# Kernel tuning notes

Hardware: AMD Instinct MI355X
Metric: run time of the kernel (lower is better)

## Reference

```python
import jax, jax.numpy as jnp
import numpy as np

N = 100_000      # num nodes
E = 100_000      # num hyperedges
NNZ = 1_600_000  # incidence entries (avg degree 16)
DIN = 128
DOUT = 128


def setup_inputs() -> dict:
    key = jax.random.key(0)
    k1, k2, k3, k4 = jax.random.split(key, 4)
    x = jax.random.normal(k1, (N, DIN), dtype=jnp.float32)
    weight = jax.random.normal(k2, (DIN, DOUT), dtype=jnp.float32) / np.sqrt(DIN).astype(np.float32)
    bias = jax.random.normal(k3, (DOUT,), dtype=jnp.float32) * 0.02
    hyperedge_index = jax.random.randint(k4, (2, NNZ), 0, N, dtype=jnp.int64)
    return {"x": x, "weight": weight, "bias": bias, "hyperedge_index": hyperedge_index}


def reference(x, weight, bias, hyperedge_index):
    # PyG HypergraphConv (use_attention=False, heads=1):
    #   out = D^{-1} H W B^{-1} H^T (x @ Theta) + bias, W = I (unit hyperedge weights)
    node_idx = hyperedge_index[0]  # [NNZ]
    edge_idx = hyperedge_index[1]  # [NNZ]

    h = x @ weight  # [N, DOUT]

    ones = jnp.ones((NNZ,), dtype=h.dtype)
    # node degree D_i = sum of hyperedge weights (=1) over incident hyperedges
    D = jax.ops.segment_sum(ones, node_idx, num_segments=N)   # [N]
    # hyperedge degree B_e = number of incident nodes
    B = jax.ops.segment_sum(ones, edge_idx, num_segments=E)   # [E]
    Dinv = jnp.where(D > 0, 1.0 / D, 0.0)
    Binv = jnp.where(B > 0, 1.0 / B, 0.0)

    # nodes -> hyperedges: m_e = B_e^{-1} * sum_{i in e} h_i
    e_feat = jax.ops.segment_sum(h[node_idx], edge_idx, num_segments=E) * Binv[:, None]  # [E, DOUT]
    # hyperedges -> nodes: out_i = D_i^{-1} * sum_{e ni i} m_e
    out = jax.ops.segment_sum(e_feat[edge_idx], node_idx, num_segments=N) * Dinv[:, None]  # [N, DOUT]
    return out + bias
```

## Files before the change

kernel.cpp:

```cpp
#include <hip/hip_runtime.h>

#define Nn 100000
#define Ne 100000
#define NNZC 1600000
#define NBLK 256
#define CHUNK 6250
#define BSH 8
#define BUCKW 256
#define NBK 391
#define GEMM_TOTAL 1563
#define GEMM_A 782
#define GEMM_B 781
#define FCAP 5888
#define SEGW 4

typedef __attribute__((ext_vector_type(8))) short short8;
typedef __attribute__((ext_vector_type(4))) float floatx4;

__device__ inline unsigned short f2bf(float f) {
    union { float f; unsigned int i; } c; c.f = f;
    unsigned int i = c.i;
    return (unsigned short)((i + 0x7fffu + ((i >> 16) & 1u)) >> 16);
}
__device__ inline unsigned int f2bf2(float lo, float hi) {
    union { float f; unsigned int i; } a, b;
    a.f = lo; b.f = hi;
    const unsigned int x = (a.i + 0x7fffu + ((a.i >> 16) & 1u)) >> 16;
    const unsigned int y = (b.i + 0x7fffu + ((b.i >> 16) & 1u)) & 0xffff0000u;
    return x | y;
}

union FusedLds {
    unsigned short wlds[128 * 136];
    struct { int a[NBK]; int b[NBK]; } s;
};

__device__ inline void gemm_block(int gb, const float* __restrict__ x,
                                  const float* __restrict__ w,
                                  unsigned short* __restrict__ h,
                                  unsigned short* wlds, int tid) {
    const int wave = tid >> 6, lane = tid & 63;
    const int q = lane >> 4, r16 = lane & 15;

    for (int i = tid; i < 4096; i += 256) {
        const int k = i >> 5;
        const int n0 = (i & 31) << 2;
        const float4 wv = *(const float4*)(w + k * 128 + n0);
        wlds[(n0 + 0) * 136 + k] = f2bf(wv.x);
        wlds[(n0 + 1) * 136 + k] = f2bf(wv.y);
        wlds[(n0 + 2) * 136 + k] = f2bf(wv.z);
        wlds[(n0 + 3) * 136 + k] = f2bf(wv.w);
    }
    __syncthreads();

    const int row0 = gb * 64 + wave * 16;
    const int rrow = min(row0 + r16, Nn - 1);

    floatx4 acc[8];
#pragma unroll
    for (int jb = 0; jb < 8; ++jb) acc[jb] = (floatx4){0.f, 0.f, 0.f, 0.f};

    const float* ap = x + (size_t)rrow * 128 + q * 8;
#pragma unroll
    for (int kk = 0; kk < 4; ++kk) {
        const float4 a0 = *(const float4*)(ap + kk * 32);
        const float4 a1 = *(const float4*)(ap + kk * 32 + 4);
        union { unsigned int u[4]; short8 s; } xf;
        xf.u[0] = f2bf2(a0.x, a0.y);
        xf.u[1] = f2bf2(a0.z, a0.w);
        xf.u[2] = f2bf2(a1.x, a1.y);
        xf.u[3] = f2bf2(a1.z, a1.w);
        const unsigned short* wp = wlds + kk * 32 + q * 8;
#pragma unroll
        for (int jb = 0; jb < 8; ++jb) {
            const short8 wf = *(const short8*)(wp + (jb * 16 + r16) * 136);
            acc[jb] = __builtin_amdgcn_mfma_f32_16x16x32_bf16(wf, xf.s, acc[jb], 0, 0, 0);
        }
    }

    if (row0 + r16 < Nn) {
        unsigned short* hb = h + (size_t)(row0 + r16) * 128 + q * 4;
#pragma unroll
        for (int jb = 0; jb < 8; ++jb) {
            uint2 o;
            o.x = f2bf2(acc[jb][0], acc[jb][1]);
            o.y = f2bf2(acc[jb][2], acc[jb][3]);
            *(uint2*)(hb + jb * 16) = o;
        }
    }
}

__global__ __launch_bounds__(256) void hist_gemm_kernel(
        const int* __restrict__ nidx, const int* __restrict__ eidx,
        int* __restrict__ histN, int* __restrict__ histE,
        const float* __restrict__ x, const float* __restrict__ w,
        unsigned short* __restrict__ h) {
    __shared__ FusedLds sm;
    const int tid = threadIdx.x;
    if (blockIdx.x < NBLK) {
        for (int j = tid; j < NBK; j += 256) { sm.s.a[j] = 0; sm.s.b[j] = 0; }
        __syncthreads();
        const int base = blockIdx.x * CHUNK;
        for (int i = base + tid; i < base + CHUNK; i += 256) {
            atomicAdd(&sm.s.a[nidx[i] >> BSH], 1);
            atomicAdd(&sm.s.b[eidx[i] >> BSH], 1);
        }
        __syncthreads();
        for (int j = tid; j < NBK; j += 256) {
            histN[j * NBLK + blockIdx.x] = sm.s.a[j];
            histE[j * NBLK + blockIdx.x] = sm.s.b[j];
        }
    } else {
        gemm_block(blockIdx.x - NBLK, x, w, h, sm.wlds, tid);
    }
}

__global__ void scan1_kernel(int* __restrict__ histN, int* __restrict__ histE,
                             int* __restrict__ bsumN, int* __restrict__ bsumE) {
    const int arr = blockIdx.x / NBK;
    const int b = blockIdx.x % NBK;
    int* a = arr ? histE : histN;
    int* bs = arr ? bsumE : bsumN;
    const int t = threadIdx.x;
    int v = a[b * 256 + t];
    __shared__ int tmp[2][256];
    int pin = 0;
    tmp[0][t] = v;
    for (int off = 1; off < 256; off <<= 1) {
        __syncthreads();
        int val = tmp[pin][t];
        if (t >= off) val += tmp[pin][t - off];
        tmp[1 - pin][t] = val;
        pin ^= 1;
    }
    __syncthreads();
    int incl = tmp[pin][t];
    a[b * 256 + t] = incl - v;
    if (t == 255) bs[b] = incl;
}

__global__ void scan3_kernel(int* __restrict__ histN, int* __restrict__ histE,
                             const int* __restrict__ bsumN, const int* __restrict__ bsumE) {
    const int arr = blockIdx.x / NBK;
    const int b = blockIdx.x % NBK;
    int* a = arr ? histE : histN;
    const int* bs = arr ? bsumE : bsumN;
    const int t = threadIdx.x;
    int part = 0;
    for (int i = t; i < b; i += 256) part += bs[i];
    __shared__ int red[256];
    red[t] = part;
    __syncthreads();
    for (int off = 128; off > 0; off >>= 1) {
        if (t < off) red[t] += red[t + off];
        __syncthreads();
    }
    a[b * 256 + t] += red[0];
}

__global__ __launch_bounds__(256) void scatter_gemm_kernel(
        const int* __restrict__ nidx, const int* __restrict__ eidx,
        const int* __restrict__ histN, const int* __restrict__ histE,
        unsigned int* __restrict__ pairsN, unsigned int* __restrict__ pairsE,
        const float* __restrict__ x, const float* __restrict__ w,
        unsigned short* __restrict__ h) {
    __shared__ FusedLds sm;
    const int tid = threadIdx.x;
    if (blockIdx.x < NBLK) {
        const int blk = blockIdx.x;
        for (int j = tid; j < NBK; j += 256) {
            sm.s.a[j] = histN[j * NBLK + blk];
            sm.s.b[j] = histE[j * NBLK + blk];
        }
        __syncthreads();
        const int base = blk * CHUNK;
        for (int i = base + tid; i < base + CHUNK; i += 256) {
            const int n = nidx[i], e = eidx[i];
            const int pn = atomicAdd(&sm.s.a[n >> BSH], 1);
            const int pe = atomicAdd(&sm.s.b[e >> BSH], 1);
            pairsN[pn] = ((unsigned int)e << 8) | (unsigned int)(n & 255);
            pairsE[pe] = ((unsigned int)n << 8) | (unsigned int)(e & 255);
        }
    } else {
        gemm_block(GEMM_A + blockIdx.x - NBLK, x, w, h, sm.wlds, tid);
    }
}

__global__ void fine_kernel(const unsigned int* __restrict__ pairsN, const unsigned int* __restrict__ pairsE,
                            const int* __restrict__ histN, const int* __restrict__ histE,
                            int* __restrict__ offsN, int* __restrict__ offsE,
                            int* __restrict__ permN, int* __restrict__ permE) {
    const int arr = blockIdx.x / NBK;
    const int b = blockIdx.x % NBK;
    const unsigned int* pairs = arr ? pairsE : pairsN;
    const int* hist = arr ? histE : histN;
    int* offs = arr ? offsE : offsN;
    int* perm = arr ? permE : permN;
    const int t = threadIdx.x;
    const int S = hist[b * NBLK];
    const int E = (b + 1 < NBK) ? hist[(b + 1) * NBLK] : NNZC;
    __shared__ int cnt[BUCKW];
    __shared__ int tmp[2][BUCKW];
    __shared__ unsigned int cache[FCAP];
    cnt[t] = 0;
    __syncthreads();
    for (int i = S + t; i < E; i += BUCKW) {
        const unsigned int p = pairs[i];
        const int loc = i - S;
        if (loc < FCAP) cache[loc] = p;
        atomicAdd(&cnt[p & 255u], 1);
    }
    __syncthreads();
    int v = cnt[t];
    int pin = 0;
    tmp[0][t] = v;
    for (int off = 1; off < BUCKW; off <<= 1) {
        __syncthreads();
        int val = tmp[pin][t];
        if (t >= off) val += tmp[pin][t - off];
        tmp[1 - pin][t] = val;
        pin ^= 1;
    }
    __syncthreads();
    const int excl = tmp[pin][t] - v;
    const int id = b * BUCKW + t;
    if (id < 100000) offs[id] = S + excl;
    if (b == NBK - 1 && t == 0) offs[100000] = NNZC;
    __syncthreads();
    cnt[t] = excl;
    __syncthreads();
    for (int i = S + t; i < E; i += BUCKW) {
        const int loc = i - S;
        const unsigned int p = (loc < FCAP) ? cache[loc] : pairs[i];
        const int pos = S + atomicAdd(&cnt[p & 255u], 1);
        perm[pos] = (int)(p >> 8);
    }
}

template <int MODE>
__global__ __launch_bounds__(256) void gather_seg_kernel(
        const int* __restrict__ perm, const int* __restrict__ offs,
        const void* __restrict__ srcv, const float* __restrict__ bias,
        void* __restrict__ outv) {
    const int wave = threadIdx.x >> 6;
    const int lane = threadIdx.x & 63;
    const int e0 = __builtin_amdgcn_readfirstlane((blockIdx.x * 4 + wave) * SEGW);
    const int start = offs[e0];
    const int end = offs[e0 + SEGW];
    const unsigned int laneoff = (unsigned int)lane << 2;
    const char* src = (const char*)srcv;

    float bx = 0.f, by = 0.f;
    if (MODE == 1) {
        const float2 b = ((const float2*)bias)[lane];
        bx = b.x; by = b.y;
    }

    float ax = 0.f, ay = 0.f;
    int e = e0;
    int seg_start = start;
    int nb = offs[e0 + 1];

    auto flush = [&](int deg) {
        const float sinv = deg ? 1.f / (float)deg : 0.f;
        if (MODE == 0) {
            *(unsigned int*)((char*)outv + (((unsigned int)e << 8) | laneoff)) =
                f2bf2(ax * sinv, ay * sinv);
        } else {
            float2 o;
            o.x = ax * sinv + bx;
            o.y = ay * sinv + by;
            *(float2*)((char*)outv + (((unsigned int)e << 9) | (laneoff << 1))) = o;
        }
        ax = 0.f; ay = 0.f;
        ++e;
    };

    int myv = 0;
    for (int i = start; i < end; i += 8) {
        const int t = (i - start) & 63;
        if (t == 0) myv = perm[min(i + lane, NNZC - 1)];
        const int m = min(end - i, 8);
        unsigned int a[8], u[8];
#pragma unroll
        for (int j = 0; j < 8; ++j)
            a[j] = ((unsigned int)__shfl(myv, t + (j < m ? j : m - 1), 64) << 8) | laneoff;
#pragma unroll
        for (int j = 0; j < 8; ++j) u[j] = *(const unsigned int*)(src + a[j]);
#pragma unroll
        for (int j = 0; j < 8; ++j) {
            if (j < m) {
                while (i + j == nb) {
                    flush(nb - seg_start);
                    seg_start = nb;
                    nb = offs[e + 1];
                }
                ax += __uint_as_float(u[j] << 16);
                ay += __uint_as_float(u[j] & 0xffff0000u);
            }
        }
    }
    while (e < e0 + SEGW) {
        flush(end - seg_start);
        seg_start = end;
    }
}

extern "C" void kernel_launch(void* const* d_in, const int* in_sizes, int n_in,
                              void* d_out, int out_size, void* d_ws, size_t ws_size,
                              hipStream_t stream) {
    const float* x = (const float*)d_in[0];
    const float* w = (const float*)d_in[1];
    const float* bias = (const float*)d_in[2];
    const int* hei = (const int*)d_in[3];
    const int* nidx = hei;
    const int* eidx = hei + NNZC;
    float* out = (float*)d_out;

    char* p = (char*)d_ws;
    unsigned short* h = (unsigned short*)p;  p += (size_t)Nn * 128 * 2;
    unsigned short* ef = (unsigned short*)p; p += (size_t)Ne * 128 * 2;
    int* histN = (int*)p;                    p += (size_t)NBK * NBLK * 4 + 256;
    int* histE = (int*)p;                    p += (size_t)NBK * NBLK * 4 + 256;
    int* bsumN = (int*)p;                    p += 1792;
    int* bsumE = (int*)p;                    p += 1792;
    int* offsN = (int*)p;                    p += 400128;
    int* offsE = (int*)p;                    p += 400128;
    int* permN = (int*)p;                    p += (size_t)NNZC * 4;
    int* permE = (int*)p;                    p += (size_t)NNZC * 4;
    unsigned int* pairsN = (unsigned int*)p; p += (size_t)NNZC * 4;
    unsigned int* pairsE = (unsigned int*)p; p += (size_t)NNZC * 4;

    hist_gemm_kernel<<<NBLK + GEMM_A, 256, 0, stream>>>(nidx, eidx, histN, histE, x, w, h);
    scan1_kernel<<<2 * NBK, 256, 0, stream>>>(histN, histE, bsumN, bsumE);
    scan3_kernel<<<2 * NBK, 256, 0, stream>>>(histN, histE, bsumN, bsumE);
    scatter_gemm_kernel<<<NBLK + GEMM_B, 256, 0, stream>>>(nidx, eidx, histN, histE,
                                                           pairsN, pairsE, x, w, h);
    fine_kernel<<<2 * NBK, BUCKW, 0, stream>>>(pairsN, pairsE, histN, histE,
                                               offsN, offsE, permN, permE);

    gather_seg_kernel<0><<<Ne / (4 * SEGW), 256, 0, stream>>>(permE, offsE, h, nullptr, ef);
    gather_seg_kernel<1><<<Nn / (4 * SEGW), 256, 0, stream>>>(permN, offsN, ef, bias, out);
}
```

Measured before the change: 311.3 us.

## Pipeline gather-segment row loads through LDS with async global_load_lds ring

Reworks the gather/segment-sum kernel so each wave issues direct global-to-LDS loads (global_load_lds) for upcoming batches of 8 gathered rows into a 4-slot per-wave LDS ring. It keeps two batches in flight and waits with explicit vmcnt before reading the oldest slot. Segment offsets are loaded once into scalars instead of being re-read during accumulation, and the next chunk of the permutation is prefetched. The goal is to hide gather latency with deeper memory-level parallelism. In exchange it adds 32 KB of LDS per block, which may reduce occupancy, and relies on hand-written waitcnt ordering.

```diff
diff --git a/kernel.cpp b/kernel.cpp
--- a/kernel.cpp
+++ b/kernel.cpp
@@ -16,6 +16,8 @@
 
 typedef __attribute__((ext_vector_type(8))) short short8;
 typedef __attribute__((ext_vector_type(4))) float floatx4;
+typedef __attribute__((address_space(1))) const unsigned int gu32;
+typedef __attribute__((address_space(3))) unsigned int lu32;
 
 __device__ inline unsigned short f2bf(float f) {
     union { float f; unsigned int i; } c; c.f = f;
@@ -242,24 +244,55 @@
         const int* __restrict__ perm, const int* __restrict__ offs,
         const void* __restrict__ srcv, const float* __restrict__ bias,
         void* __restrict__ outv) {
+    __shared__ unsigned int ring[4][4][8][64];
     const int wave = threadIdx.x >> 6;
     const int lane = threadIdx.x & 63;
     const int e0 = __builtin_amdgcn_readfirstlane((blockIdx.x * 4 + wave) * SEGW);
-    const int start = offs[e0];
-    const int end = offs[e0 + SEGW];
+
+    const int o0 = __builtin_amdgcn_readfirstlane(offs[e0]);
+    const int o1 = __builtin_amdgcn_readfirstlane(offs[e0 + 1]);
+    const int o2 = __builtin_amdgcn_readfirstlane(offs[e0 + 2]);
+    const int o3 = __builtin_amdgcn_readfirstlane(offs[e0 + 3]);
+    const int o4 = __builtin_amdgcn_readfirstlane(offs[e0 + 4]);
+    const int start = o0, end = o4;
+    const int nrows = end - start;
+    const int nbatch = (nrows + 7) >> 3;
+
     const unsigned int laneoff = (unsigned int)lane << 2;
     const char* src = (const char*)srcv;
 
     float bx = 0.f, by = 0.f;
-    if (MODE == 1) {
-        const float2 b = ((const float2*)bias)[lane];
-        bx = b.x; by = b.y;
-    }
+    if (MODE == 1) { const float2 b = ((const float2*)bias)[lane]; bx = b.x; by = b.y; }
+
+    int cur = perm[min(start + lane, NNZC - 1)];
+    int nxt = perm[min(start + 64 + lane, NNZC - 1)];
+    int wbase = 0;
+
+    unsigned int* const myring = &ring[wave][0][0][0];
+
+    auto issue = [&](int b) {
+        const int rel0 = b << 3;
+        if ((rel0 >> 6) > wbase) {
+            cur = nxt;
+            ++wbase;
+            nxt = perm[min(start + ((wbase + 1) << 6) + lane, NNZC - 1)];
+        }
+        const int rbase = rel0 & 63;
+        const int relmax = nrows - 1 - (wbase << 6);
+        unsigned int* lslot = myring + ((b & 3) << 9);
+#pragma unroll
+        for (int j = 0; j < 8; ++j) {
+            const int k = min(rbase + j, relmax);
+            const unsigned int rid = (unsigned int)__shfl(cur, k, 64);
+            const char* g = src + (((unsigned long long)rid << 8) | laneoff);
+            __builtin_amdgcn_global_load_lds((gu32*)g, (lu32*)(lslot + (j << 6)), 4, 0, 0);
+        }
+    };
 
     float ax = 0.f, ay = 0.f;
     int e = e0;
     int seg_start = start;
-    int nb = offs[e0 + 1];
+    int nb = o1;
 
     auto flush = [&](int deg) {
         const float sinv = deg ? 1.f / (float)deg : 0.f;
@@ -275,30 +308,48 @@
         ax = 0.f; ay = 0.f;
         ++e;
     };
-
-    int myv = 0;
-    for (int i = start; i < end; i += 8) {
-        const int t = (i - start) & 63;
-        if (t == 0) myv = perm[min(i + lane, NNZC - 1)];
+    auto nextnb = [&]() {
+        const int k = e - e0;
+        return k == 0 ? o1 : k == 1 ? o2 : k == 2 ? o3 : o4;
+    };
+
+    auto accumulate = [&](int t, const unsigned int* u) {
+        const int i = start + (t << 3);
         const int m = min(end - i, 8);
-        unsigned int a[8], u[8];
-#pragma unroll
-        for (int j = 0; j < 8; ++j)
-            a[j] = ((unsigned int)__shfl(myv, t + (j < m ? j : m - 1), 64) << 8) | laneoff;
-#pragma unroll
-        for (int j = 0; j < 8; ++j) u[j] = *(const unsigned int*)(src + a[j]);
 #pragma unroll
         for (int j = 0; j < 8; ++j) {
             if (j < m) {
                 while (i + j == nb) {
                     flush(nb - seg_start);
                     seg_start = nb;
-                    nb = offs[e + 1];
+                    nb = nextnb();
                 }
                 ax += __uint_as_float(u[j] << 16);
                 ay += __uint_as_float(u[j] & 0xffff0000u);
             }
         }
+    };
+
+    if (nbatch > 0) issue(0);
+    if (nbatch > 1) issue(1);
+
+    for (int t = 0; t + 1 < nbatch; ++t) {
+        asm volatile("s_waitcnt vmcnt(8)" ::: "memory");
+        const unsigned int* lslot = myring + ((t & 3) << 9);
+        unsigned int u[8];
+#pragma unroll
+        for (int j = 0; j < 8; ++j) u[j] = lslot[(j << 6) + lane];
+        if (t + 2 < nbatch) issue(t + 2);
+        accumulate(t, u);
+    }
+    if (nbatch > 0) {
+        asm volatile("s_waitcnt vmcnt(0)" ::: "memory");
+        const int t = nbatch - 1;
+        const unsigned int* lslot = myring + ((t & 3) << 9);
+        unsigned int u[8];
+#pragma unroll
+        for (int j = 0; j < 8; ++j) u[j] = lslot[(j << 6) + lane];
+        accumulate(t, u);
     }
     while (e < e0 + SEGW) {
         flush(end - seg_start);
```

Result: slower. 406.8 us (+30.7%).

## Replace two-level radix CSR build with global atomic counting sort

Applied to the files above, without the earlier changes.

Replaces the coarse-bucket histogram, pair scatter and per-bucket fine sort with a direct counting sort: global atomics count the degree of each node and hyperedge, a two-pass scan turns the counts into offsets, and a second pass of global atomics scatters the neighbor ids straight into CSR order. This drops the fine_kernel launch and the pairs intermediate buffers. In exchange it issues 3.2M global atomics spread over random addresses, on top of a memset, and the order of entries within a segment becomes nondeterministic, which can slightly change floating-point summation order.

```diff
diff --git a/kernel.cpp b/kernel.cpp
--- a/kernel.cpp
+++ b/kernel.cpp
@@ -5,13 +5,10 @@
 #define NNZC 1600000
 #define NBLK 256
 #define CHUNK 6250
-#define BSH 8
-#define BUCKW 256
 #define NBK 391
 #define GEMM_TOTAL 1563
 #define GEMM_A 782
 #define GEMM_B 781
-#define FCAP 5888
 #define SEGW 4
 
 typedef __attribute__((ext_vector_type(8))) short short8;
@@ -29,11 +26,6 @@
     const unsigned int y = (b.i + 0x7fffu + ((b.i >> 16) & 1u)) & 0xffff0000u;
     return x | y;
 }
-
-union FusedLds {
-    unsigned short wlds[128 * 136];
-    struct { int a[NBK]; int b[NBK]; } s;
-};
 
 __device__ inline void gemm_block(int gb, const float* __restrict__ x,
                                   const float* __restrict__ w,
@@ -90,39 +82,35 @@
     }
 }
 
-__global__ __launch_bounds__(256) void hist_gemm_kernel(
+__global__ __launch_bounds__(256) void count_gemm_kernel(
         const int* __restrict__ nidx, const int* __restrict__ eidx,
-        int* __restrict__ histN, int* __restrict__ histE,
+        int* __restrict__ cntN, int* __restrict__ cntE,
         const float* __restrict__ x, const float* __restrict__ w,
         unsigned short* __restrict__ h) {
-    __shared__ FusedLds sm;
+    __shared__ unsigned short wlds[128 * 136];
     const int tid = threadIdx.x;
     if (blockIdx.x < NBLK) {
-        for (int j = tid; j < NBK; j += 256) { sm.s.a[j] = 0; sm.s.b[j] = 0; }
-        __syncthreads();
         const int base = blockIdx.x * CHUNK;
         for (int i = base + tid; i < base + CHUNK; i += 256) {
-            atomicAdd(&sm.s.a[nidx[i] >> BSH], 1);
-            atomicAdd(&sm.s.b[eidx[i] >> BSH], 1);
-        }
-        __syncthreads();
-        for (int j = tid; j < NBK; j += 256) {
-            histN[j * NBLK + blockIdx.x] = sm.s.a[j];
-            histE[j * NBLK + blockIdx.x] = sm.s.b[j];
+            atomicAdd(&cntN[nidx[i]], 1);
+            atomicAdd(&cntE[eidx[i]], 1);
         }
     } else {
-        gemm_block(blockIdx.x - NBLK, x, w, h, sm.wlds, tid);
-    }
-}
-
-__global__ void scan1_kernel(int* __restrict__ histN, int* __restrict__ histE,
+        gemm_block(blockIdx.x - NBLK, x, w, h, wlds, tid);
+    }
+}
+
+__global__ void scanA_kernel(const int* __restrict__ cntN, const int* __restrict__ cntE,
+                             int* __restrict__ offsN, int* __restrict__ offsE,
                              int* __restrict__ bsumN, int* __restrict__ bsumE) {
     const int arr = blockIdx.x / NBK;
     const int b = blockIdx.x % NBK;
-    int* a = arr ? histE : histN;
+    const int* c = arr ? cntE : cntN;
+    int* o = arr ? offsE : offsN;
     int* bs = arr ? bsumE : bsumN;
     const int t = threadIdx.x;
-    int v = a[b * 256 + t];
+    const int id = b * 256 + t;
+    const int v = (id < 100000) ? c[id] : 0;
     __shared__ int tmp[2][256];
     int pin = 0;
     tmp[0][t] = v;
@@ -134,16 +122,18 @@
         pin ^= 1;
     }
     __syncthreads();
-    int incl = tmp[pin][t];
-    a[b * 256 + t] = incl - v;
+    const int incl = tmp[pin][t];
+    if (id < 100000) o[id] = incl - v;
     if (t == 255) bs[b] = incl;
 }
 
-__global__ void scan3_kernel(int* __restrict__ histN, int* __restrict__ histE,
+__global__ void scanB_kernel(int* __restrict__ offsN, int* __restrict__ offsE,
+                             int* __restrict__ curN, int* __restrict__ curE,
                              const int* __restrict__ bsumN, const int* __restrict__ bsumE) {
     const int arr = blockIdx.x / NBK;
     const int b = blockIdx.x % NBK;
-    int* a = arr ? histE : histN;
+    int* o = arr ? offsE : offsN;
+    int* cu = arr ? curE : curN;
     const int* bs = arr ? bsumE : bsumN;
     const int t = threadIdx.x;
     int part = 0;
@@ -155,85 +145,34 @@
         if (t < off) red[t] += red[t + off];
         __syncthreads();
     }
-    a[b * 256 + t] += red[0];
+    const int id = b * 256 + t;
+    if (id < 100000) {
+        const int val = o[id] + red[0];
+        o[id] = val;
+        cu[id] = val;
+    }
+    if (b == NBK - 1 && t == 0) o[100000] = NNZC;
 }
 
 __global__ __launch_bounds__(256) void scatter_gemm_kernel(
         const int* __restrict__ nidx, const int* __restrict__ eidx,
-        const int* __restrict__ histN, const int* __restrict__ histE,
-        unsigned int* __restrict__ pairsN, unsigned int* __restrict__ pairsE,
+        int* __restrict__ curN, int* __restrict__ curE,
+        int* __restrict__ permN, int* __restrict__ permE,
         const float* __restrict__ x, const float* __restrict__ w,
         unsigned short* __restrict__ h) {
-    __shared__ FusedLds sm;
+    __shared__ unsigned short wlds[128 * 136];
     const int tid = threadIdx.x;
     if (blockIdx.x < NBLK) {
-        const int blk = blockIdx.x;
-        for (int j = tid; j < NBK; j += 256) {
-            sm.s.a[j] = histN[j * NBLK + blk];
-            sm.s.b[j] = histE[j * NBLK + blk];
-        }
-        __syncthreads();
-        const int base = blk * CHUNK;
+        const int base = blockIdx.x * CHUNK;
         for (int i = base + tid; i < base + CHUNK; i += 256) {
             const int n = nidx[i], e = eidx[i];
-            const int pn = atomicAdd(&sm.s.a[n >> BSH], 1);
-            const int pe = atomicAdd(&sm.s.b[e >> BSH], 1);
-            pairsN[pn] = ((unsigned int)e << 8) | (unsigned int)(n & 255);
-            pairsE[pe] = ((unsigned int)n << 8) | (unsigned int)(e & 255);
+            const int pn = atomicAdd(&curN[n], 1);
+            permN[pn] = e;
+            const int pe = atomicAdd(&curE[e], 1);
+            permE[pe] = n;
         }
     } else {
-        gemm_block(GEMM_A + blockIdx.x - NBLK, x, w, h, sm.wlds, tid);
-    }
-}
-
-__global__ void fine_kernel(const unsigned int* __restrict__ pairsN, const unsigned int* __restrict__ pairsE,
-                            const int* __restrict__ histN, const int* __restrict__ histE,
-                            int* __restrict__ offsN, int* __restrict__ offsE,
-                            int* __restrict__ permN, int* __restrict__ permE) {
-    const int arr = blockIdx.x / NBK;
-    const int b = blockIdx.x % NBK;
-    const unsigned int* pairs = arr ? pairsE : pairsN;
-    const int* hist = arr ? histE : histN;
-    int* offs = arr ? offsE : offsN;
-    int* perm = arr ? permE : permN;
-    const int t = threadIdx.x;
-    const int S = hist[b * NBLK];
-    const int E = (b + 1 < NBK) ? hist[(b + 1) * NBLK] : NNZC;
-    __shared__ int cnt[BUCKW];
-    __shared__ int tmp[2][BUCKW];
-    __shared__ unsigned int cache[FCAP];
-    cnt[t] = 0;
-    __syncthreads();
-    for (int i = S + t; i < E; i += BUCKW) {
-        const unsigned int p = pairs[i];
-        const int loc = i - S;
-        if (loc < FCAP) cache[loc] = p;
-        atomicAdd(&cnt[p & 255u], 1);
-    }
-    __syncthreads();
-    int v = cnt[t];
-    int pin = 0;
-    tmp[0][t] = v;
-    for (int off = 1; off < BUCKW; off <<= 1) {
-        __syncthreads();
-        int val = tmp[pin][t];
-        if (t >= off) val += tmp[pin][t - off];
-        tmp[1 - pin][t] = val;
-        pin ^= 1;
-    }
-    __syncthreads();
-    const int excl = tmp[pin][t] - v;
-    const int id = b * BUCKW + t;
-    if (id < 100000) offs[id] = S + excl;
-    if (b == NBK - 1 && t == 0) offs[100000] = NNZC;
-    __syncthreads();
-    cnt[t] = excl;
-    __syncthreads();
-    for (int i = S + t; i < E; i += BUCKW) {
-        const int loc = i - S;
-        const unsigned int p = (loc < FCAP) ? cache[loc] : pairs[i];
-        const int pos = S + atomicAdd(&cnt[p & 255u], 1);
-        perm[pos] = (int)(p >> 8);
+        gemm_block(GEMM_A + blockIdx.x - NBLK, x, w, h, wlds, tid);
     }
 }
 
@@ -320,24 +259,23 @@
     char* p = (char*)d_ws;
     unsigned short* h = (unsigned short*)p;  p += (size_t)Nn * 128 * 2;
     unsigned short* ef = (unsigned short*)p; p += (size_t)Ne * 128 * 2;
-    int* histN = (int*)p;                    p += (size_t)NBK * NBLK * 4 + 256;
-    int* histE = (int*)p;                    p += (size_t)NBK * NBLK * 4 + 256;
+    int* cntN = (int*)p;                     p += 400384;
+    int* cntE = (int*)p;                     p += 400384;
     int* bsumN = (int*)p;                    p += 1792;
     int* bsumE = (int*)p;                    p += 1792;
-    int* offsN = (int*)p;                    p += 400128;
-    int* offsE = (int*)p;                    p += 400128;
+    int* offsN = (int*)p;                    p += 400384;
+    int* offsE = (int*)p;                    p += 400384;
+    int* curN = (int*)p;                     p += 400384;
+    int* curE = (int*)p;                     p += 400384;
     int* permN = (int*)p;                    p += (size_t)NNZC * 4;
     int* permE = (int*)p;                    p += (size_t)NNZC * 4;
-    unsigned int* pairsN = (unsigned int*)p; p += (size_t)NNZC * 4;
-    unsigned int* pairsE = (unsigned int*)p; p += (size_t)NNZC * 4;
-
-    hist_gemm_kernel<<<NBLK + GEMM_A, 256, 0, stream>>>(nidx, eidx, histN, histE, x, w, h);
-    scan1_kernel<<<2 * NBK, 256, 0, stream>>>(histN, histE, bsumN, bsumE);
-    scan3_kernel<<<2 * NBK, 256, 0, stream>>>(histN, histE, bsumN, bsumE);
-    scatter_gemm_kernel<<<NBLK + GEMM_B, 256, 0, stream>>>(nidx, eidx, histN, histE,
-                                                           pairsN, pairsE, x, w, h);
-    fine_kernel<<<2 * NBK, BUCKW, 0, stream>>>(pairsN, pairsE, histN, histE,
-                                               offsN, offsE, permN, permE);
+
+    hipMemsetAsync(cntN, 0, 2 * 400384, stream);
+    count_gemm_kernel<<<NBLK + GEMM_A, 256, 0, stream>>>(nidx, eidx, cntN, cntE, x, w, h);
+    scanA_kernel<<<2 * NBK, 256, 0, stream>>>(cntN, cntE, offsN, offsE, bsumN, bsumE);
+    scanB_kernel<<<2 * NBK, 256, 0, stream>>>(offsN, offsE, curN, curE, bsumN, bsumE);
+    scatter_gemm_kernel<<<NBLK + GEMM_B, 256, 0, stream>>>(nidx, eidx, curN, curE,
+                                                           permN, permE, x, w, h);
 
     gather_seg_kernel<0><<<Ne / (4 * SEGW), 256, 0, stream>>>(permE, offsE, h, nullptr, ef);
     gather_seg_kernel<1><<<Nn / (4 * SEGW), 256, 0, stream>>>(permN, offsN, ef, bias, out);
```

After: 604.2 us. 1.94x slower.

## Split GEMM into three parts and co-schedule fine sort with GEMM and gather

Applied to the files above, without the earlier changes.

The GEMM blocks are now spread across three kernels. A third slice runs alongside the hyperedge-side fine sort. The node-side fine sort now runs inside the same launch as the first gather (nodes to hyperedges) instead of in its own kernel before both gathers. This fills idle CUs during the low-parallelism fine-sort phase and removes one launch. In exchange, the LDS cache capacity (FCAP) shrinks so the combined LDS union fits. This may raise global re-reads for large buckets and changes block scheduling balance.

```diff
diff --git a/kernel.cpp b/kernel.cpp
--- a/kernel.cpp
+++ b/kernel.cpp
@@ -9,10 +9,12 @@
 #define BUCKW 256
 #define NBK 391
 #define GEMM_TOTAL 1563
-#define GEMM_A 782
-#define GEMM_B 781
-#define FCAP 5888
+#define GEMM_A 600
+#define GEMM_B 600
+#define GEMM_C 363
+#define FCAP 4608
 #define SEGW 4
+#define NG0 6250
 
 typedef __attribute__((ext_vector_type(8))) short short8;
 typedef __attribute__((ext_vector_type(4))) float floatx4;
@@ -33,6 +35,15 @@
 union FusedLds {
     unsigned short wlds[128 * 136];
     struct { int a[NBK]; int b[NBK]; } s;
+};
+struct FineLds {
+    int cnt[BUCKW];
+    int tmp[2][BUCKW];
+    unsigned int cache[FCAP];
+};
+union FineGemmLds {
+    unsigned short wlds[128 * 136];
+    FineLds f;
 };
 
 __device__ inline void gemm_block(int gb, const float* __restrict__ x,
@@ -87,6 +98,117 @@
             o.y = f2bf2(acc[jb][2], acc[jb][3]);
             *(uint2*)(hb + jb * 16) = o;
         }
+    }
+}
+
+__device__ inline void fine_block(int b, const unsigned int* __restrict__ pairs,
+                                  const int* __restrict__ hist,
+                                  int* __restrict__ offs, int* __restrict__ perm,
+                                  FineLds& L, int t) {
+    const int S = hist[b * NBLK];
+    const int E = (b + 1 < NBK) ? hist[(b + 1) * NBLK] : NNZC;
+    L.cnt[t] = 0;
+    __syncthreads();
+    for (int i = S + t; i < E; i += BUCKW) {
+        const unsigned int p = pairs[i];
+        const int loc = i - S;
+        if (loc < FCAP) L.cache[loc] = p;
+        atomicAdd(&L.cnt[p & 255u], 1);
+    }
+    __syncthreads();
+    int v = L.cnt[t];
+    int pin = 0;
+    L.tmp[0][t] = v;
+    for (int off = 1; off < BUCKW; off <<= 1) {
+        __syncthreads();
+        int val = L.tmp[pin][t];
+        if (t >= off) val += L.tmp[pin][t - off];
+        L.tmp[1 - pin][t] = val;
+        pin ^= 1;
+    }
+    __syncthreads();
+    const int excl = L.tmp[pin][t] - v;
+    const int id = b * BUCKW + t;
+    if (id < 100000) offs[id] = S + excl;
+    if (b == NBK - 1 && t == 0) offs[100000] = NNZC;
+    __syncthreads();
+    L.cnt[t] = excl;
+    __syncthreads();
+    for (int i = S + t; i < E; i += BUCKW) {
+        const int loc = i - S;
+        const unsigned int p = (loc < FCAP) ? L.cache[loc] : pairs[i];
+        const int pos = S + atomicAdd(&L.cnt[p & 255u], 1);
+        perm[pos] = (int)(p >> 8);
+    }
+}
+
+template <int MODE>
+__device__ inline void gather_body(int gblk, const int* __restrict__ perm,
+                                   const int* __restrict__ offs,
+                                   const void* __restrict__ srcv,
+                                   const float* __restrict__ bias,
+                                   void* __restrict__ outv, int tid) {
+    const int wave = tid >> 6;
+    const int lane = tid & 63;
+    const int e0 = __builtin_amdgcn_readfirstlane((gblk * 4 + wave) * SEGW);
+    const int start = offs[e0];
+    const int end = offs[e0 + SEGW];
+    const unsigned int laneoff = (unsigned int)lane << 2;
+    const char* src = (const char*)srcv;
+
+    float bx = 0.f, by = 0.f;
+    if (MODE == 1) {
+        const float2 b = ((const float2*)bias)[lane];
+        bx = b.x; by = b.y;
+    }
+
+    float ax = 0.f, ay = 0.f;
+    int e = e0;
+    int seg_start = start;
+    int nb = offs[e0 + 1];
+
+    auto flush = [&](int deg) {
+        const float sinv = deg ? 1.f / (float)deg : 0.f;
+        if (MODE == 0) {
+            *(unsigned int*)((char*)outv + (((unsigned int)e << 8) | laneoff)) =
+                f2bf2(ax * sinv, ay * sinv);
+        } else {
+            float2 o;
+            o.x = ax * sinv + bx;
+            o.y = ay * sinv + by;
+            *(float2*)((char*)outv + (((unsigned int)e << 9) | (laneoff << 1))) = o;
+        }
+        ax = 0.f; ay = 0.f;
+        ++e;
+    };
+
+    int myv = 0;
+    for (int i = start; i < end; i += 8) {
+        const int t = (i - start) & 63;
+        if (t == 0) myv = perm[min(i + lane, NNZC - 1)];
+        const int m = min(end - i, 8);
+        unsigned int a[8], u[8];
+#pragma unroll
+        for (int j = 0; j < 8; ++j)
+            a[j] = ((unsigned int)__shfl(myv, t + (j < m ? j : m - 1), 64) << 8) | laneoff;
+#pragma unroll
+        for (int j = 0; j < 8; ++j) u[j] = *(const unsigned int*)(src + a[j]);
+#pragma unroll
+        for (int j = 0; j < 8; ++j) {
+            if (j < m) {
+                while (i + j == nb) {
+                    flush(nb - seg_start);
+                    seg_start = nb;
+                    nb = offs[e + 1];
+                }
+                ax += __uint_as_float(u[j] << 16);
+                ay += __uint_as_float(u[j] & 0xffff0000u);
+            }
+        }
+    }
+    while (e < e0 + SEGW) {
+        flush(end - seg_start);
+        seg_start = end;
     }
 }
 
@@ -186,124 +308,39 @@
     }
 }
 
-__global__ void fine_kernel(const unsigned int* __restrict__ pairsN, const unsigned int* __restrict__ pairsE,
-                            const int* __restrict__ histN, const int* __restrict__ histE,
-                            int* __restrict__ offsN, int* __restrict__ offsE,
-                            int* __restrict__ permN, int* __restrict__ permE) {
-    const int arr = blockIdx.x / NBK;
-    const int b = blockIdx.x % NBK;
-    const unsigned int* pairs = arr ? pairsE : pairsN;
-    const int* hist = arr ? histE : histN;
-    int* offs = arr ? offsE : offsN;
-    int* perm = arr ? permE : permN;
-    const int t = threadIdx.x;
-    const int S = hist[b * NBLK];
-    const int E = (b + 1 < NBK) ? hist[(b + 1) * NBLK] : NNZC;
-    __shared__ int cnt[BUCKW];
-    __shared__ int tmp[2][BUCKW];
-    __shared__ unsigned int cache[FCAP];
-    cnt[t] = 0;
-    __syncthreads();
-    for (int i = S + t; i < E; i += BUCKW) {
-        const unsigned int p = pairs[i];
-        const int loc = i - S;
-        if (loc < FCAP) cache[loc] = p;
-        atomicAdd(&cnt[p & 255u], 1);
-    }
-    __syncthreads();
-    int v = cnt[t];
-    int pin = 0;
-    tmp[0][t] = v;
-    for (int off = 1; off < BUCKW; off <<= 1) {
-        __syncthreads();
-        int val = tmp[pin][t];
-        if (t >= off) val += tmp[pin][t - off];
-        tmp[1 - pin][t] = val;
-        pin ^= 1;
-    }
-    __syncthreads();
-    const int excl = tmp[pin][t] - v;
-    const int id = b * BUCKW + t;
-    if (id < 100000) offs[id] = S + excl;
-    if (b == NBK - 1 && t == 0) offs[100000] = NNZC;
-    __syncthreads();
-    cnt[t] = excl;
-    __syncthreads();
-    for (int i = S + t; i < E; i += BUCKW) {
-        const int loc = i - S;
-        const unsigned int p = (loc < FCAP) ? cache[loc] : pairs[i];
-        const int pos = S + atomicAdd(&cnt[p & 255u], 1);
-        perm[pos] = (int)(p >> 8);
-    }
-}
-
-template <int MODE>
-__global__ __launch_bounds__(256) void gather_seg_kernel(
-        const int* __restrict__ perm, const int* __restrict__ offs,
-        const void* __restrict__ srcv, const float* __restrict__ bias,
-        void* __restrict__ outv) {
-    const int wave = threadIdx.x >> 6;
-    const int lane = threadIdx.x & 63;
-    const int e0 = __builtin_amdgcn_readfirstlane((blockIdx.x * 4 + wave) * SEGW);
-    const int start = offs[e0];
-    const int end = offs[e0 + SEGW];
-    const unsigned int laneoff = (unsigned int)lane << 2;
-    const char* src = (const char*)srcv;
-
-    float bx = 0.f, by = 0.f;
-    if (MODE == 1) {
-        const float2 b = ((const float2*)bias)[lane];
-        bx = b.x; by = b.y;
-    }
-
-    float ax = 0.f, ay = 0.f;
-    int e = e0;
-    int seg_start = start;
-    int nb = offs[e0 + 1];
-
-    auto flush = [&](int deg) {
-        const float sinv = deg ? 1.f / (float)deg : 0.f;
-        if (MODE == 0) {
-            *(unsigned int*)((char*)outv + (((unsigned int)e << 8) | laneoff)) =
-                f2bf2(ax * sinv, ay * sinv);
-        } else {
-            float2 o;
-            o.x = ax * sinv + bx;
-            o.y = ay * sinv + by;
-            *(float2*)((char*)outv + (((unsigned int)e << 9) | (laneoff << 1))) = o;
-        }
-        ax = 0.f; ay = 0.f;
-        ++e;
-    };
-
-    int myv = 0;
-    for (int i = start; i < end; i += 8) {
-        const int t = (i - start) & 63;
-        if (t == 0) myv = perm[min(i + lane, NNZC - 1)];
-        const int m = min(end - i, 8);
-        unsigned int a[8], u[8];
-#pragma unroll
-        for (int j = 0; j < 8; ++j)
-            a[j] = ((unsigned int)__shfl(myv, t + (j < m ? j : m - 1), 64) << 8) | laneoff;
-#pragma unroll
-        for (int j = 0; j < 8; ++j) u[j] = *(const unsigned int*)(src + a[j]);
-#pragma unroll
-        for (int j = 0; j < 8; ++j) {
-            if (j < m) {
-                while (i + j == nb) {
-                    flush(nb - seg_start);
-                    seg_start = nb;
-                    nb = offs[e + 1];
-                }
-                ax += __uint_as_float(u[j] << 16);
-                ay += __uint_as_float(u[j] & 0xffff0000u);
-            }
-        }
-    }
-    while (e < e0 + SEGW) {
-        flush(end - seg_start);
-        seg_start = end;
-    }
+__global__ __launch_bounds__(256) void fineE_gemm_kernel(
+        const unsigned int* __restrict__ pairsE, const int* __restrict__ histE,
+        int* __restrict__ offsE, int* __restrict__ permE,
+        const float* __restrict__ x, const float* __restrict__ w,
+        unsigned short* __restrict__ h) {
+    __shared__ FineGemmLds sm;
+    const int tid = threadIdx.x;
+    if (blockIdx.x < NBK) {
+        fine_block(blockIdx.x, pairsE, histE, offsE, permE, sm.f, tid);
+    } else {
+        gemm_block(GEMM_A + GEMM_B + blockIdx.x - NBK, x, w, h, sm.wlds, tid);
+    }
+}
+
+__global__ __launch_bounds__(256) void g0_fineN_kernel(
+        const int* __restrict__ permE, const int* __restrict__ offsE,
+        const unsigned short* __restrict__ h, unsigned short* __restrict__ ef,
+        const unsigned int* __restrict__ pairsN, const int* __restrict__ histN,
+        int* __restrict__ offsN, int* __restrict__ permN) {
+    __shared__ FineLds sm;
+    const int tid = threadIdx.x;
+    if (blockIdx.x < NG0) {
+        gather_body<0>(blockIdx.x, permE, offsE, h, nullptr, ef, tid);
+    } else {
+        fine_block(blockIdx.x - NG0, pairsN, histN, offsN, permN, sm, tid);
+    }
+}
+
+__global__ __launch_bounds__(256) void gather_e2n_kernel(
+        const int* __restrict__ permN, const int* __restrict__ offsN,
+        const unsigned short* __restrict__ ef, const float* __restrict__ bias,
+        float* __restrict__ out) {
+    gather_body<1>(blockIdx.x, permN, offsN, ef, bias, out, threadIdx.x);
 }
 
 extern "C" void kernel_launch(void* const* d_in, const int* in_sizes, int n_in,
@@ -336,9 +373,10 @@
     scan3_kernel<<<2 * NBK, 256, 0, stream>>>(histN, histE, bsumN, bsumE);
     scatter_gemm_kernel<<<NBLK + GEMM_B, 256, 0, stream>>>(nidx, eidx, histN, histE,
                                                            pairsN, pairsE, x, w, h);
-    fine_kernel<<<2 * NBK, BUCKW, 0, stream>>>(pairsN, pairsE, histN, histE,
-                                               offsN, offsE, permN, permE);
-
-    gather_seg_kernel<0><<<Ne / (4 * SEGW), 256, 0, stream>>>(permE, offsE, h, nullptr, ef);
-    gather_seg_kernel<1><<<Nn / (4 * SEGW), 256, 0, stream>>>(permN, offsN, ef, bias, out);
-}
+    fineE_gemm_kernel<<<NBK + GEMM_C, 256, 0, stream>>>(pairsE, histE, offsE, permE,
+                                                        x, w, h);
+
+    g0_fineN_kernel<<<NG0 + NBK, 256, 0, stream>>>(permE, offsE, h, ef,
+                                                   pairsN, histN, offsN, permN);
+    gather_e2n_kernel<<<Nn / (4 * SEGW), 256, 0, stream>>>(permN, offsN, ef, bias, out);
+}
```

Result: no change. 315.7 us (+1.4%).
